# Kernel optimization log

Hardware: AMD Instinct MI355X
Metric: run time of the kernel (lower is better)

The kernel has to match this reference:

```python
import jax, jax.numpy as jnp
import numpy as np

F_CNT, V_CNT = 1024, 512
H, W = 192, 192
FX, FY = 200.0, 200.0
CX, CY = W / 2.0, H / 2.0
EPS = 1e-8


def quat_to_rot(q):
    # WXYZ quaternion -> rotation matrix, with normalization.
    q = q / (jnp.linalg.norm(q, axis=-1, keepdims=True) + EPS)
    w, x, y, z = q[..., 0], q[..., 1], q[..., 2], q[..., 3]
    return jnp.stack([
        jnp.stack([1 - 2 * (y * y + z * z), 2 * (x * y - w * z), 2 * (x * z + w * y)], -1),
        jnp.stack([2 * (x * y + w * z), 1 - 2 * (x * x + z * z), 2 * (y * z - w * x)], -1),
        jnp.stack([2 * (x * z - w * y), 2 * (y * z + w * x), 1 - 2 * (x * x + y * y)], -1),
    ], -2)


def rot_to_quat(R):
    # Branchless rotation matrix -> WXYZ quaternion.
    m00, m11, m22 = R[..., 0, 0], R[..., 1, 1], R[..., 2, 2]
    qw = 0.5 * jnp.sqrt(jnp.maximum(EPS, 1 + m00 + m11 + m22))
    qx = 0.5 * jnp.sqrt(jnp.maximum(EPS, 1 + m00 - m11 - m22))
    qy = 0.5 * jnp.sqrt(jnp.maximum(EPS, 1 - m00 + m11 - m22))
    qz = 0.5 * jnp.sqrt(jnp.maximum(EPS, 1 - m00 - m11 + m22))
    qx = jnp.copysign(qx, R[..., 2, 1] - R[..., 1, 2])
    qy = jnp.copysign(qy, R[..., 0, 2] - R[..., 2, 0])
    qz = jnp.copysign(qz, R[..., 1, 0] - R[..., 0, 1])
    return jnp.stack([qw, qx, qy, qz], -1)


def get_face_coord(a, b, c):
    # Per-face orthonormal frame (columns = x,y,z axes) and centroid.
    t = (a + b + c) / 3.0
    e1, e2 = b - a, c - a
    x = e1 / (jnp.linalg.norm(e1, axis=-1, keepdims=True) + EPS)
    n = jnp.cross(e1, e2)
    z = n / (jnp.linalg.norm(n, axis=-1, keepdims=True) + EPS)
    y = jnp.cross(z, x)
    return jnp.stack([x, y, z], -1), t


def render_gaussians(means, rot_qs, scales, colors, opac):
    # Differentiable 3DGS-style render: project, build 2D conics, depth-sorted
    # alpha compositing over all gaussians per pixel, white background.
    Rn = quat_to_rot(rot_qs)                      # [F,3,3]
    M = Rn * scales[:, None, :]                   # R @ diag(s)
    cov3 = M @ jnp.swapaxes(M, -1, -2)            # [F,3,3]
    X, Y, Z = means[:, 0], means[:, 1], means[:, 2]
    valid = (Z > 0.2).astype(means.dtype)
    Zc = jnp.maximum(Z, 0.2)
    mx = FX * X / Zc + CX
    my = FY * Y / Zc + CY
    zero = jnp.zeros_like(Zc)
    J = jnp.stack([
        jnp.stack([FX / Zc, zero, -FX * X / (Zc * Zc)], -1),
        jnp.stack([zero, FY / Zc, -FY * Y / (Zc * Zc)], -1),
    ], -2)                                        # [F,2,3]
    cov2 = J @ cov3 @ jnp.swapaxes(J, -1, -2)     # [F,2,2]
    a = cov2[:, 0, 0] + 0.3                       # low-pass dilation (3DGS)
    b = cov2[:, 0, 1]
    c = cov2[:, 1, 1] + 0.3
    det = jnp.maximum(a * c - b * b, EPS)
    conA, conB, conC = c / det, -b / det, a / det
    ys, xs = jnp.meshgrid(jnp.arange(H, dtype=means.dtype),
                          jnp.arange(W, dtype=means.dtype), indexing='ij')
    px, py = xs.reshape(-1), ys.reshape(-1)       # [HW]
    dx = px[None, :] - mx[:, None]                # [F,HW]
    dy = py[None, :] - my[:, None]
    power = -0.5 * (conA[:, None] * dx * dx + conC[:, None] * dy * dy) - conB[:, None] * dx * dy
    alpha = jnp.clip(opac[:, None] * jnp.exp(jnp.minimum(power, 0.0)), 0.0, 0.99) * valid[:, None]
    order = jnp.argsort(Zc)                       # front-to-back
    alpha = alpha[order]
    cols = colors[order]
    T = jnp.cumprod(1.0 - alpha, axis=0)
    T_excl = jnp.concatenate([jnp.ones_like(T[:1]), T[:-1]], axis=0)
    w = alpha * T_excl                            # [F,HW]
    img = jnp.einsum('fp,fc->cp', w, cols) + (1.0 - jnp.sum(w, 0))[None, :]
    return img.reshape(colors.shape[1], H, W)


def setup_inputs() -> dict:
    ks = jax.random.split(jax.random.key(0), 8)
    vp = jax.random.normal(ks[0], (V_CNT, 3), jnp.float32) * 0.5
    vp = vp.at[:, 2].add(5.0)  # put the mesh in front of the camera
    return {
        'img': jax.random.uniform(ks[1], (3, H, W), jnp.float32),
        'mask': jax.random.uniform(ks[2], (H, W), jnp.float32),
        'vertex_positions': vp,
        'faces': jax.random.randint(ks[3], (F_CNT, 3), 0, V_CNT, jnp.int32),
        'gp_rot_qs': jax.random.normal(ks[4], (F_CNT, 4), jnp.float32),
        'gp_log_scales': jax.random.normal(ks[5], (F_CNT, 3), jnp.float32) * 0.1 - 3.0,
        'gp_colors': jax.random.uniform(ks[6], (F_CNT, 3), jnp.float32),
        'gp_log_opacities': jnp.zeros((F_CNT, 1), jnp.float32),
    }


def reference(img, mask, vertex_positions, faces, gp_rot_qs, gp_log_scales,
              gp_colors, gp_log_opacities):
    vps_a = vertex_positions[faces[:, 0]]
    vps_b = vertex_positions[faces[:, 1]]
    vps_c = vertex_positions[faces[:, 2]]
    face_rs, face_ts = get_face_coord(vps_a, vps_b, vps_c)      # [F,3,3],[F,3]
    gp_scales = jnp.exp(gp_log_scales)
    gp_rot_mats = quat_to_rot(gp_rot_qs)
    # rows = scaled columns of the rotation (exactly as the torch code stacks)
    gp_rs = jnp.stack([gp_rot_mats[:, :, 0] * gp_scales[:, 0:1],
                       gp_rot_mats[:, :, 1] * gp_scales[:, 1:2],
                       gp_rot_mats[:, :, 2] * gp_scales[:, 2:3]], -2)
    global_gp_rs = face_rs @ gp_rs                               # merge_rt, gp_t = 0
    global_gp_ts = face_ts
    global_scales = jnp.linalg.norm(global_gp_rs, axis=-2)      # column norms [F,3]
    global_rot = global_gp_rs / (global_scales[:, None, :] + EPS)
    global_qs = rot_to_quat(global_rot)
    opac = jnp.exp(gp_log_opacities)[:, 0]
    rendered = render_gaussians(global_gp_ts, global_qs, global_scales, gp_colors, opac)
    mask_ = mask[None]
    masked_img = (1.0 - mask_) + img * mask_                     # white bg composite
    rgb_loss = jnp.mean((rendered - masked_img) ** 2)
    return rendered, rgb_loss
```

## Files before the change

kernel.cpp:

```cpp
#include <hip/hip_runtime.h>
#include <hip/hip_fp16.h>
#include <math.h>

#define F_CNT 1024
#define H_IMG 192
#define W_IMG 192
#define HW (H_IMG * W_IMG)
#define EPSF 1e-8f
#define N_SEG 8
#define SEG_LEN 128
#define HALF_PX 72
#define PIX_PER_BLK 144
#define LOG2E 1.4426950408889634f

#define RCP(x) __builtin_amdgcn_rcpf(x)


__global__ __launch_bounds__(1024)
void prep_sort_kernel(const float* __restrict__ vp,
                      const int*   __restrict__ faces,
                      const float* __restrict__ rot_qs,
                      const float* __restrict__ log_scales,
                      const float* __restrict__ colors,
                      const float* __restrict__ log_opac,
                      float* __restrict__ params,
                      float* __restrict__ out)
{
    __shared__ float sp[8][F_CNT];
    __shared__ unsigned long long skv[F_CNT];

    const int f = threadIdx.x;
    if (f == 0) out[3 * HW] = 0.0f;

    const int ia = faces[3 * f + 0], ib = faces[3 * f + 1], ic = faces[3 * f + 2];
    const float Ax = vp[3 * ia + 0], Ay = vp[3 * ia + 1], Az = vp[3 * ia + 2];
    const float Bx = vp[3 * ib + 0], By = vp[3 * ib + 1], Bz = vp[3 * ib + 2];
    const float Cx = vp[3 * ic + 0], Cy = vp[3 * ic + 1], Cz = vp[3 * ic + 2];

    const float tx = (Ax + Bx + Cx) / 3.0f;
    const float ty = (Ay + By + Cy) / 3.0f;
    const float tz = (Az + Bz + Cz) / 3.0f;

    const float e1x = Bx - Ax, e1y = By - Ay, e1z = Bz - Az;
    const float e2x = Cx - Ax, e2y = Cy - Ay, e2z = Cz - Az;

    const float rn1 = RCP(sqrtf(e1x * e1x + e1y * e1y + e1z * e1z) + EPSF);
    const float ux = e1x * rn1, uy = e1y * rn1, uz = e1z * rn1;
    const float cnx = e1y * e2z - e1z * e2y;
    const float cny = e1z * e2x - e1x * e2z;
    const float cnz = e1x * e2y - e1y * e2x;
    const float rn2 = RCP(sqrtf(cnx * cnx + cny * cny + cnz * cnz) + EPSF);
    const float wxv = cnx * rn2, wyv = cny * rn2, wzv = cnz * rn2;
    const float vx = wyv * uz - wzv * uy;
    const float vy = wzv * ux - wxv * uz;
    const float vz = wxv * uy - wyv * ux;

    const float q0 = rot_qs[4 * f + 0], q1 = rot_qs[4 * f + 1];
    const float q2 = rot_qs[4 * f + 2], q3 = rot_qs[4 * f + 3];
    const float rqn = RCP(sqrtf(q0 * q0 + q1 * q1 + q2 * q2 + q3 * q3) + EPSF);
    const float qw = q0 * rqn, qx = q1 * rqn, qy = q2 * rqn, qz = q3 * rqn;
    const float R00 = 1.0f - 2.0f * (qy * qy + qz * qz);
    const float R01 = 2.0f * (qx * qy - qw * qz);
    const float R02 = 2.0f * (qx * qz + qw * qy);
    const float R10 = 2.0f * (qx * qy + qw * qz);
    const float R11 = 1.0f - 2.0f * (qx * qx + qz * qz);
    const float R12 = 2.0f * (qy * qz - qw * qx);
    const float R20 = 2.0f * (qx * qz - qw * qy);
    const float R21 = 2.0f * (qy * qz + qw * qx);
    const float R22 = 1.0f - 2.0f * (qx * qx + qy * qy);

    const float s0 = expf(log_scales[3 * f + 0]);
    const float s1 = expf(log_scales[3 * f + 1]);
    const float s2 = expf(log_scales[3 * f + 2]);

    float G00, G10, G20, G01, G11, G21, G02, G12, G22;
    {
        float c0 = s0 * R00, c1 = s1 * R01, c2 = s2 * R02;
        G00 = ux * c0 + vx * c1 + wxv * c2;
        G10 = uy * c0 + vy * c1 + wyv * c2;
        G20 = uz * c0 + vz * c1 + wzv * c2;
    }
    {
        float c0 = s0 * R10, c1 = s1 * R11, c2 = s2 * R12;
        G01 = ux * c0 + vx * c1 + wxv * c2;
        G11 = uy * c0 + vy * c1 + wyv * c2;
        G21 = uz * c0 + vz * c1 + wzv * c2;
    }
    {
        float c0 = s0 * R20, c1 = s1 * R21, c2 = s2 * R22;
        G02 = ux * c0 + vx * c1 + wxv * c2;
        G12 = uy * c0 + vy * c1 + wyv * c2;
        G22 = uz * c0 + vz * c1 + wzv * c2;
    }

    const float gs0 = sqrtf(G00 * G00 + G10 * G10 + G20 * G20);
    const float gs1 = sqrtf(G01 * G01 + G11 * G11 + G21 * G21);
    const float gs2 = sqrtf(G02 * G02 + G12 * G12 + G22 * G22);
    const float rd0 = RCP(gs0 + EPSF), rd1 = RCP(gs1 + EPSF), rd2 = RCP(gs2 + EPSF);
    const float r00 = G00 * rd0, r10 = G10 * rd0, r20 = G20 * rd0;
    const float r01 = G01 * rd1, r11 = G11 * rd1, r21 = G21 * rd1;
    const float r02 = G02 * rd2, r12 = G12 * rd2, r22 = G22 * rd2;

    const float Qw = 0.5f * sqrtf(fmaxf(EPSF, 1.0f + r00 + r11 + r22));
    const float Qx = copysignf(0.5f * sqrtf(fmaxf(EPSF, 1.0f + r00 - r11 - r22)), r21 - r12);
    const float Qy = copysignf(0.5f * sqrtf(fmaxf(EPSF, 1.0f - r00 + r11 - r22)), r02 - r20);
    const float Qz = copysignf(0.5f * sqrtf(fmaxf(EPSF, 1.0f - r00 - r11 + r22)), r10 - r01);

    const float rqn2 = RCP(sqrtf(Qw * Qw + Qx * Qx + Qy * Qy + Qz * Qz) + EPSF);
    const float pw = Qw * rqn2, px = Qx * rqn2, py = Qy * rqn2, pz = Qz * rqn2;
    const float N00 = 1.0f - 2.0f * (py * py + pz * pz);
    const float N01 = 2.0f * (px * py - pw * pz);
    const float N02 = 2.0f * (px * pz + pw * py);
    const float N10 = 2.0f * (px * py + pw * pz);
    const float N11 = 1.0f - 2.0f * (px * px + pz * pz);
    const float N12 = 2.0f * (py * pz - pw * px);
    const float N20 = 2.0f * (px * pz - pw * py);
    const float N21 = 2.0f * (py * pz + pw * px);
    const float N22 = 1.0f - 2.0f * (px * px + py * py);

    const float M00 = N00 * gs0, M01 = N01 * gs1, M02 = N02 * gs2;
    const float M10 = N10 * gs0, M11 = N11 * gs1, M12 = N12 * gs2;
    const float M20 = N20 * gs0, M21 = N21 * gs1, M22 = N22 * gs2;
    const float C00 = M00 * M00 + M01 * M01 + M02 * M02;
    const float C01 = M00 * M10 + M01 * M11 + M02 * M12;
    const float C02 = M00 * M20 + M01 * M21 + M02 * M22;
    const float C11 = M10 * M10 + M11 * M11 + M12 * M12;
    const float C12 = M10 * M20 + M11 * M21 + M12 * M22;
    const float C22 = M20 * M20 + M21 * M21 + M22 * M22;

    const float valid = (tz > 0.2f) ? 1.0f : 0.0f;
    const float Zc = fmaxf(tz, 0.2f);
    const float rZc = RCP(Zc);
    const float mx = 200.0f * tx * rZc + 96.0f;
    const float my = 200.0f * ty * rZc + 96.0f;
    const float j00 = 200.0f * rZc;
    const float j02 = -200.0f * tx * (rZc * rZc);
    const float j11 = 200.0f * rZc;
    const float j12 = -200.0f * ty * (rZc * rZc);
    const float v00 = j00 * j00 * C00 + 2.0f * j00 * j02 * C02 + j02 * j02 * C22 + 0.3f;
    const float v01 = j00 * j11 * C01 + j00 * j12 * C02 + j02 * j11 * C12 + j02 * j12 * C22;
    const float v11 = j11 * j11 * C11 + 2.0f * j11 * j12 * C12 + j12 * j12 * C22 + 0.3f;
    const float rdet = RCP(fmaxf(v00 * v11 - v01 * v01, EPSF));
    const float conA = v11 * rdet, conB = -v01 * rdet, conC = v00 * rdet;
    const float opv = expf(log_opac[f]) * valid;

    const float LA = 0.5f * LOG2E * conA;
    const float LB = LOG2E * conB;
    const float LC = 0.5f * LOG2E * conC;
    const float t4 = fmaf(-LB, LB, 4.0f * LA * LC);
    const float reach2 = 140.0f * LA * RCP(fmaxf(t4, 1e-30f));

    union { __half2 h; float f; } c01u, cbo;
    c01u.h = __floats2half2_rn(colors[3 * f + 0], colors[3 * f + 1]);
    cbo.h  = __floats2half2_rn(colors[3 * f + 2], opv);

    sp[0][f] = mx;
    sp[1][f] = my;
    sp[2][f] = reach2;
    sp[3][f] = LA;
    sp[4][f] = LB;
    sp[5][f] = LC;
    sp[6][f] = c01u.f;
    sp[7][f] = cbo.f;

    unsigned long long kv =
        ((unsigned long long)__float_as_uint(Zc) << 32) | (unsigned int)f;

    #pragma unroll
    for (int k = 2; k <= 64; k <<= 1)
        #pragma unroll
        for (int j = k >> 1; j > 0; j >>= 1) {
            const unsigned long long pk = __shfl_xor(kv, j, 64);
            const bool keep_min = (((f & k) == 0) == ((f & j) == 0));
            kv = ((pk < kv) == keep_min) ? pk : kv;
        }

    skv[f] = kv;
    __syncthreads();

    for (int k = 128; k <= F_CNT; k <<= 1) {
        for (int j = k >> 1; j >= 64; j >>= 1) {
            const int x = f ^ j;
            if (x > f) {
                const unsigned long long a  = skv[f];
                const unsigned long long bb = skv[x];
                const bool up = ((f & k) == 0);
                if (up ? (a > bb) : (a < bb)) { skv[f] = bb; skv[x] = a; }
            }
            __syncthreads();
        }
        kv = skv[f];
        #pragma unroll
        for (int j = 32; j > 0; j >>= 1) {
            const unsigned long long pk = __shfl_xor(kv, j, 64);
            const bool keep_min = (((f & k) == 0) == ((f & j) == 0));
            kv = ((pk < kv) == keep_min) ? pk : kv;
        }
        skv[f] = kv;
        __syncthreads();
    }

    const int src = (int)(skv[f] & 0xffffffffULL);
    float4* __restrict__ d4 = (float4*)params + 2 * f;
    d4[0] = make_float4(sp[0][src], sp[1][src], sp[2][src], sp[3][src]);
    d4[1] = make_float4(sp[4][src], sp[5][src], sp[6][src], sp[7][src]);
}

__global__ __launch_bounds__(512)
void render_partial_kernel(const float* __restrict__ params,
                           float* __restrict__ partials)
{
    __shared__ float4 lds4[1024];
    __shared__ float2 myr[512];
    __shared__ unsigned int hlist[8][SEG_LEN];

    const int tid  = threadIdx.x;
    const int lane = tid & 63;
    const int wv   = tid >> 6;

    const int bid = blockIdx.x;
    const int h   = bid >> 8;
    const int r   = (bid + (h ? 128 : 0)) & 255;

    {
        const float4* __restrict__ rec4 = (const float4*)params;
        const float4 a  = rec4[2 * (512 * h + tid) + 0];
        const float4 bb = rec4[2 * (512 * h + tid) + 1];
        lds4[2 * tid + 0] = a;
        lds4[2 * tid + 1] = bb;
        myr[tid] = make_float2(a.y, a.z);
    }
    __syncthreads();

    const int pb1 = r * HALF_PX;
    const int pb2 = HW / 2 + r * HALF_PX;
    const int seg_l  = wv & 3;
    const bool strip2 = (wv >= 4);
    const int pbase  = strip2 ? pb2 : pb1;

    const float ra = (float)(pbase / W_IMG);
    const float rb = (float)((pbase + HALF_PX - 1) / W_IMG);

    int nhit;
    {
        const float4 tt = ((const float4*)myr)[seg_l * 64 + lane];
        const float dmA = fmaxf(0.0f, fmaxf(ra - tt.x, tt.x - rb));
        const float dmB = fmaxf(0.0f, fmaxf(ra - tt.z, tt.z - rb));
        const bool hA = dmA * dmA <= tt.y;
        const bool hB = dmB * dmB <= tt.w;

        const unsigned long long m0 = __ballot(hA);
        const unsigned long long m1 = __ballot(hB);
        const unsigned long long lt = (1ULL << lane) - 1ULL;
        const int pos0 = __popcll(m0 & lt) + __popcll(m1 & lt);
        const int pos1 = pos0 + (hA ? 1 : 0);
        if (hA) hlist[wv][pos0] = (unsigned)(2 * lane);
        if (hB) hlist[wv][pos1] = (unsigned)(2 * lane + 1);
        nhit = __popcll(m0) + __popcll(m1);
    }
    __syncthreads();

    const int p0 = pbase + lane, p1 = pbase + 64 + lane;
    const float fx0 = (float)(p0 % W_IMG), fy0 = (float)(p0 / W_IMG);
    const float fx1 = (float)(p1 % W_IMG), fy1 = (float)(p1 / W_IMG);

    float T0 = 1.0f, R0 = 0.0f, G0 = 0.0f, B0 = 0.0f;
    float T1 = 1.0f, R1 = 0.0f, G1 = 0.0f, B1 = 0.0f;

    const float4* __restrict__ Lb = lds4 + (seg_l << 8);
    for (int i = 0; i < nhit; ++i) {
        const int rr = (int)hlist[wv][i];
        const float4 a  = Lb[2 * rr + 0];
        const float4 bb = Lb[2 * rr + 1];
        const float my = a.y;
        const float LA = a.w, LB = bb.x, LC = bb.y;
        union { float f; __half2 h; } urg, ubo;
        urg.f = bb.z;  ubo.f = bb.w;
        const float2 crg = __half22float2(urg.h);
        const float2 cbo = __half22float2(ubo.h);
        const float  cb  = cbo.x, opv = cbo.y;

        {
            const float dx = fx0 - a.x, dy = fy0 - my;
            const float t  = fmaf(LB, dy, LA * dx);
            const float u2 = (LC * dy) * dy;
            const float n  = -fmaf(t, dx, u2);
            const float e2 = exp2f(fminf(n, 0.0f));
            const float al = fminf(opv * e2, 0.99f);
            const float w  = al * T0;
            R0 = fmaf(w, crg.x, R0); G0 = fmaf(w, crg.y, G0); B0 = fmaf(w, cb, B0);
            T0 -= w;
        }
        {
            const float dx = fx1 - a.x, dy = fy1 - my;
            const float t  = fmaf(LB, dy, LA * dx);
            const float u2 = (LC * dy) * dy;
            const float n  = -fmaf(t, dx, u2);
            const float e2 = exp2f(fminf(n, 0.0f));
            const float al = fminf(opv * e2, 0.99f);
            const float w  = al * T1;
            R1 = fmaf(w, crg.x, R1); G1 = fmaf(w, crg.y, G1); B1 = fmaf(w, cb, B1);
            T1 -= w;
        }
    }

    float4* __restrict__ part = (float4*)partials;
    const int gseg = 4 * h + seg_l;
    const int base = (r * N_SEG + gseg) * PIX_PER_BLK + (strip2 ? HALF_PX : 0);
    part[base + lane] = make_float4(R0, G0, B0, T0);
    if (lane < 8)
        part[base + 64 + lane] = make_float4(R1, G1, B1, T1);
}

__global__ __launch_bounds__(256)
void combine_kernel(const float* __restrict__ partials,
                    const float* __restrict__ img,
                    const float* __restrict__ mask,
                    float* __restrict__ out)
{
    __shared__ float lossb[PIX_PER_BLK];

    const int tid = threadIdx.x;
    const int c   = blockIdx.x;
    const int pb1 = c * HALF_PX;
    const int pb2 = HW / 2 + c * HALF_PX;

    float lsum = 0.0f;
    if (tid < PIX_PER_BLK) {
        const float4* __restrict__ part = (const float4*)partials;
        float R = 0.0f, G = 0.0f, B = 0.0f, Tt = 1.0f;
        #pragma unroll
        for (int s = 0; s < N_SEG; ++s) {
            const float4 cc = part[(c * N_SEG + s) * PIX_PER_BLK + tid];
            R += Tt * cc.x; G += Tt * cc.y; B += Tt * cc.z;
            Tt *= cc.w;
        }
        const float bg = Tt;
        const float o0 = R + bg, o1 = G + bg, o2 = B + bg;
        const int p = (tid < HALF_PX) ? (pb1 + tid) : (pb2 + tid - HALF_PX);
        out[p]          = o0;
        out[HW + p]     = o1;
        out[2 * HW + p] = o2;

        const float m = mask[p];
        const float base = 1.0f - m;
        const float e0 = o0 - (base + img[p] * m);
        const float e1 = o1 - (base + img[HW + p] * m);
        const float e2 = o2 - (base + img[2 * HW + p] * m);
        lsum = e0 * e0 + e1 * e1 + e2 * e2;
    }

    if (tid < PIX_PER_BLK) lossb[tid] = lsum;
    __syncthreads();
    if (tid < 64) {
        float s = lossb[tid] + lossb[tid + 64] + (tid < 16 ? lossb[tid + 128] : 0.0f);
        #pragma unroll
        for (int off = 32; off > 0; off >>= 1) s += __shfl_down(s, off);
        if (tid == 0)
            atomicAdd(out + 3 * HW, s * (1.0f / (float)(3 * HW)));
    }
}

extern "C" void kernel_launch(void* const* d_in, const int* in_sizes, int n_in,
                              void* d_out, int out_size, void* d_ws, size_t ws_size,
                              hipStream_t stream)
{
    const float* img        = (const float*)d_in[0];
    const float* mask       = (const float*)d_in[1];
    const float* vp         = (const float*)d_in[2];
    const int*   faces      = (const int*)d_in[3];
    const float* rot_qs     = (const float*)d_in[4];
    const float* log_scales = (const float*)d_in[5];
    const float* colors     = (const float*)d_in[6];
    const float* log_opac   = (const float*)d_in[7];
    float* out      = (float*)d_out;
    float* params   = (float*)d_ws;
    float* partials = (float*)d_ws + 8192;

    prep_sort_kernel<<<1, F_CNT, 0, stream>>>(vp, faces, rot_qs, log_scales,
                                              colors, log_opac, params, out);
    render_partial_kernel<<<512, 512, 0, stream>>>(params, partials);
    combine_kernel<<<256, 256, 0, stream>>>(partials, img, mask, out);
}
```

Before: 100.9 us.

## Iterate ballot hit masks directly and prefetch gaussian records two ahead

Removes the LDS hit-list compaction and the block-wide barrier that followed it. Each wave now walks its two 64-bit ballot masks in ascending order using count-trailing-zeros, which keeps the original depth order. The loop also software-pipelines the LDS loads of the next gaussian record while the current one is composited, to hide LDS latency. The cost is extra registers for the prefetched records and more scalar mask-handling logic per iteration.

```diff
diff --git a/kernel.cpp b/kernel.cpp
--- a/kernel.cpp
+++ b/kernel.cpp
@@ -212,7 +212,6 @@
 {
     __shared__ float4 lds4[1024];
     __shared__ float2 myr[512];
-    __shared__ unsigned int hlist[8][SEG_LEN];
 
     const int tid  = threadIdx.x;
     const int lane = tid & 63;
@@ -241,24 +240,17 @@
     const float ra = (float)(pbase / W_IMG);
     const float rb = (float)((pbase + HALF_PX - 1) / W_IMG);
 
-    int nhit;
+    unsigned long long mA, mB;
     {
-        const float4 tt = ((const float4*)myr)[seg_l * 64 + lane];
-        const float dmA = fmaxf(0.0f, fmaxf(ra - tt.x, tt.x - rb));
-        const float dmB = fmaxf(0.0f, fmaxf(ra - tt.z, tt.z - rb));
-        const bool hA = dmA * dmA <= tt.y;
-        const bool hB = dmB * dmB <= tt.w;
-
-        const unsigned long long m0 = __ballot(hA);
-        const unsigned long long m1 = __ballot(hB);
-        const unsigned long long lt = (1ULL << lane) - 1ULL;
-        const int pos0 = __popcll(m0 & lt) + __popcll(m1 & lt);
-        const int pos1 = pos0 + (hA ? 1 : 0);
-        if (hA) hlist[wv][pos0] = (unsigned)(2 * lane);
-        if (hB) hlist[wv][pos1] = (unsigned)(2 * lane + 1);
-        nhit = __popcll(m0) + __popcll(m1);
-    }
-    __syncthreads();
+        const float2 t0 = myr[seg_l * 128 + lane];
+        const float2 t1 = myr[seg_l * 128 + 64 + lane];
+        const float dm0 = fmaxf(0.0f, fmaxf(ra - t0.x, t0.x - rb));
+        const float dm1 = fmaxf(0.0f, fmaxf(ra - t1.x, t1.x - rb));
+        const bool h0 = dm0 * dm0 <= t0.y;
+        const bool h1 = dm1 * dm1 <= t1.y;
+        mA = __ballot(h0);
+        mB = __ballot(h1);
+    }
 
     const int p0 = pbase + lane, p1 = pbase + 64 + lane;
     const float fx0 = (float)(p0 % W_IMG), fy0 = (float)(p0 / W_IMG);
@@ -267,11 +259,37 @@
     float T0 = 1.0f, R0 = 0.0f, G0 = 0.0f, B0 = 0.0f;
     float T1 = 1.0f, R1 = 0.0f, G1 = 0.0f, B1 = 0.0f;
 
-    const float4* __restrict__ Lb = lds4 + (seg_l << 8);
-    for (int i = 0; i < nhit; ++i) {
-        const int rr = (int)hlist[wv][i];
-        const float4 a  = Lb[2 * rr + 0];
-        const float4 bb = Lb[2 * rr + 1];
+    const float4* __restrict__ Lb = lds4 + (seg_l << 7) * 2;
+    unsigned long long mm = mA;
+    bool ph2 = false;
+
+#define NEXT_R(dst) do {                                              \
+        if (mm == 0ULL && !ph2) { mm = mB; ph2 = true; }              \
+        if (mm != 0ULL) {                                             \
+            const int _b = (int)__builtin_ctzll(mm);                  \
+            mm &= mm - 1ULL;                                          \
+            (dst) = _b + (ph2 ? 64 : 0);                              \
+        } else (dst) = -1;                                            \
+    } while (0)
+
+    int rA, rB;
+    NEXT_R(rA);
+    rB = -1;
+    float4 aP0, bP0, aP1, bP1;
+    if (rA >= 0) {
+        aP0 = Lb[2 * rA + 0]; bP0 = Lb[2 * rA + 1];
+        NEXT_R(rB);
+        if (rB >= 0) { aP1 = Lb[2 * rB + 0]; bP1 = Lb[2 * rB + 1]; }
+    }
+
+    while (rA >= 0) {
+        const float4 a  = aP0;
+        const float4 bb = bP0;
+        aP0 = aP1; bP0 = bP1;
+        int rN = -1;
+        if (rB >= 0) NEXT_R(rN);
+        if (rN >= 0) { aP1 = Lb[2 * rN + 0]; bP1 = Lb[2 * rN + 1]; }
+
         const float my = a.y;
         const float LA = a.w, LB = bb.x, LC = bb.y;
         union { float f; __half2 h; } urg, ubo;
@@ -302,7 +320,10 @@
             R1 = fmaf(w, crg.x, R1); G1 = fmaf(w, crg.y, G1); B1 = fmaf(w, cb, B1);
             T1 -= w;
         }
-    }
+
+        rA = rB; rB = rN;
+    }
+#undef NEXT_R
 
     float4* __restrict__ part = (float4*)partials;
     const int gseg = 4 * h + seg_l;
```

After: 107.5 us. +6.5%, slower.

## Split render into 16 depth segments of 64 gaussians across 1024 blocks

Applied to the files above, without the earlier changes.

Each render block now processes 256 gaussians, split into four wave segments of 64, instead of 512 split into four segments of 128. The grid doubles to 1024 blocks, and each thread culls one gaussian instead of two. The goal is more parallelism and shorter serial compositing loops per wave, which should improve load balance. In exchange there are twice as many partial records, and the combine kernel must composite 16 segments, which raises partial memory traffic.

```diff
diff --git a/kernel.cpp b/kernel.cpp
--- a/kernel.cpp
+++ b/kernel.cpp
@@ -7,8 +7,8 @@
 #define W_IMG 192
 #define HW (H_IMG * W_IMG)
 #define EPSF 1e-8f
-#define N_SEG 8
-#define SEG_LEN 128
+#define N_SEG 16
+#define SEG_LEN 64
 #define HALF_PX 72
 #define PIX_PER_BLK 144
 #define LOG2E 1.4426950408889634f
@@ -210,8 +210,8 @@
 void render_partial_kernel(const float* __restrict__ params,
                            float* __restrict__ partials)
 {
-    __shared__ float4 lds4[1024];
-    __shared__ float2 myr[512];
+    __shared__ float4 lds4[512];
+    __shared__ float2 myr[256];
     __shared__ unsigned int hlist[8][SEG_LEN];
 
     const int tid  = threadIdx.x;
@@ -219,15 +219,16 @@
     const int wv   = tid >> 6;
 
     const int bid = blockIdx.x;
-    const int h   = bid >> 8;
-    const int r   = (bid + (h ? 128 : 0)) & 255;
+    const int q   = bid >> 8;
+    const int r   = (bid + q * 64) & 255;
 
     {
         const float4* __restrict__ rec4 = (const float4*)params;
-        const float4 a  = rec4[2 * (512 * h + tid) + 0];
-        const float4 bb = rec4[2 * (512 * h + tid) + 1];
-        lds4[2 * tid + 0] = a;
-        lds4[2 * tid + 1] = bb;
+        lds4[tid] = rec4[q * 512 + tid];
+    }
+    __syncthreads();
+    if (tid < 256) {
+        const float4 a = lds4[2 * tid];
         myr[tid] = make_float2(a.y, a.z);
     }
     __syncthreads();
@@ -243,20 +244,14 @@
 
     int nhit;
     {
-        const float4 tt = ((const float4*)myr)[seg_l * 64 + lane];
-        const float dmA = fmaxf(0.0f, fmaxf(ra - tt.x, tt.x - rb));
-        const float dmB = fmaxf(0.0f, fmaxf(ra - tt.z, tt.z - rb));
-        const bool hA = dmA * dmA <= tt.y;
-        const bool hB = dmB * dmB <= tt.w;
-
-        const unsigned long long m0 = __ballot(hA);
-        const unsigned long long m1 = __ballot(hB);
+        const float2 t0 = myr[seg_l * 64 + lane];
+        const float dm0 = fmaxf(0.0f, fmaxf(ra - t0.x, t0.x - rb));
+        const bool h0 = dm0 * dm0 <= t0.y;
+        const unsigned long long m0 = __ballot(h0);
         const unsigned long long lt = (1ULL << lane) - 1ULL;
-        const int pos0 = __popcll(m0 & lt) + __popcll(m1 & lt);
-        const int pos1 = pos0 + (hA ? 1 : 0);
-        if (hA) hlist[wv][pos0] = (unsigned)(2 * lane);
-        if (hB) hlist[wv][pos1] = (unsigned)(2 * lane + 1);
-        nhit = __popcll(m0) + __popcll(m1);
+        const int pos0 = __popcll(m0 & lt);
+        if (h0) hlist[wv][pos0] = (unsigned)lane;
+        nhit = __popcll(m0);
     }
     __syncthreads();
 
@@ -267,7 +262,7 @@
     float T0 = 1.0f, R0 = 0.0f, G0 = 0.0f, B0 = 0.0f;
     float T1 = 1.0f, R1 = 0.0f, G1 = 0.0f, B1 = 0.0f;
 
-    const float4* __restrict__ Lb = lds4 + (seg_l << 8);
+    const float4* __restrict__ Lb = lds4 + (seg_l << 7);
     for (int i = 0; i < nhit; ++i) {
         const int rr = (int)hlist[wv][i];
         const float4 a  = Lb[2 * rr + 0];
@@ -305,7 +300,7 @@
     }
 
     float4* __restrict__ part = (float4*)partials;
-    const int gseg = 4 * h + seg_l;
+    const int gseg = 4 * q + seg_l;
     const int base = (r * N_SEG + gseg) * PIX_PER_BLK + (strip2 ? HALF_PX : 0);
     part[base + lane] = make_float4(R0, G0, B0, T0);
     if (lane < 8)
@@ -379,6 +374,6 @@
 
     prep_sort_kernel<<<1, F_CNT, 0, stream>>>(vp, faces, rot_qs, log_scales,
                                               colors, log_opac, params, out);
-    render_partial_kernel<<<512, 512, 0, stream>>>(params, partials);
+    render_partial_kernel<<<1024, 512, 0, stream>>>(params, partials);
     combine_kernel<<<256, 256, 0, stream>>>(partials, img, mask, out);
 }
```

Result: faster. 97.93 us (median of 2 runs) (-2.9%).
